# Kernel tuning notes

Hardware: AMD Instinct MI355X
Metric: run time of the kernel (lower is better)

## Reference

```python
import jax, jax.numpy as jnp
import numpy as np

N, D, E = 50000, 128, 800000


def setup_inputs() -> dict:
    key = jax.random.key(0)
    ks = jax.random.split(key, 12)
    x0 = jax.random.normal(ks[0], (N, D), dtype=jnp.float32)
    x1 = jax.random.normal(ks[1], (N, D), dtype=jnp.float32)
    edge_index = jax.random.randint(ks[2], (2, E), 0, N, dtype=jnp.int64)
    s = 0.05
    W1 = jax.random.normal(ks[3], (D, D), dtype=jnp.float32) * s
    b1 = jax.random.normal(ks[4], (D,), dtype=jnp.float32) * s
    W2 = jax.random.normal(ks[5], (D, D), dtype=jnp.float32) * s
    b2 = jax.random.normal(ks[6], (D,), dtype=jnp.float32) * s
    a1_w = jax.random.normal(ks[7], (D,), dtype=jnp.float32) * s
    a1_b = jax.random.normal(ks[8], (), dtype=jnp.float32) * s
    a2_w = jax.random.normal(ks[9], (D,), dtype=jnp.float32) * s
    a2_b = jax.random.normal(ks[10], (), dtype=jnp.float32) * s
    return {"x0": x0, "x1": x1, "edge_index": edge_index,
            "W1": W1, "b1": b1, "W2": W2, "b2": b2,
            "a1_w": a1_w, "a1_b": a1_b, "a2_w": a2_w, "a2_b": a2_b}


def reference(x0, x1, edge_index, W1, b1, W2, b2, a1_w, a1_b, a2_w, a2_b):
    # LeakyReLU(0.2) applied to both projections
    lrelu = lambda v: jnp.where(v >= 0, v, 0.2 * v)
    x0_i = lrelu(x0 @ W1.T + b1)          # [N, D]
    x0_j = lrelu(x0 @ W2.T + b2)          # [N, D]
    a1 = x0_i @ a1_w + a1_b               # [N]
    a2 = x0_j @ a2_w + a2_b               # [N]
    src, dst = edge_index[0], edge_index[1]
    # sigmoid(a_1 + a_2.T) evaluated only at the sparse edge indices
    att = jax.nn.sigmoid(a1[src] + a2[dst])            # [E]
    msg = att[:, None] * x0_j[dst]                     # [E, D]
    out = jax.ops.segment_sum(msg, src, num_segments=x0.shape[0])  # sparse.mm
    return out + x0
```

## Files before the change

### kernel.cpp

```cpp
#include <hip/hip_runtime.h>
#include <hip/hip_bf16.h>

typedef unsigned int u32;
typedef unsigned short u16;

#define DIM 128
#define LWS 136
#define CHUNK 2048

typedef __bf16 bfrag __attribute__((ext_vector_type(8)));
typedef float  facc  __attribute__((ext_vector_type(4)));

__device__ __forceinline__ float2 bfpair(u32 u) {
    union { u32 i; float f; } lo, hi;
    lo.i = (u & 0xFFFFu) << 16;
    hi.i = u & 0xFFFF0000u;
    return make_float2(lo.f, hi.f);
}
__device__ __forceinline__ float bf1(u16 h) {
    union { u32 i; float f; } a; a.i = ((u32)h) << 16; return a.f;
}
__device__ __forceinline__ u16 f2bf(float f) {
    __hip_bfloat16 h = __float2bfloat16(f);
    return *reinterpret_cast<u16*>(&h);
}
__device__ __forceinline__ u32 packbf(float x, float y) {
    return (u32)f2bf(x) | ((u32)f2bf(y) << 16);
}
__device__ __forceinline__ float ldfr(const void* p, int i, bool isbf) {
    return isbf ? bf1(((const u16*)p)[i]) : ((const float*)p)[i];
}

__global__ __launch_bounds__(64) void sniff_kernel(const u32* __restrict__ x0w,
                                                   const int* __restrict__ eiw,
                                                   int* __restrict__ flags) {
    int l = threadIdx.x;
    u32 w = x0w[l];
    u32 ef = (w >> 7) & 0xFF;
    bool inr = (ef >= 99 && ef <= 141);
    unsigned long long m1 = __ballot(inr);
    bool zodd = (eiw[2 * l + 1] == 0);
    unsigned long long m2 = __ballot(zodd);
    if (l == 0) {
        flags[0] = (__popcll(m1) >= 48) ? 1 : 0;
        flags[1] = (__popcll(m2) >= 32) ? 1 : 0;
    }
}

__global__ __launch_bounds__(256) void cvt_kernel(
    const float* __restrict__ x0, const float* __restrict__ W1,
    const float* __restrict__ W2, u16* __restrict__ x0c, u16* __restrict__ Wc,
    const int* __restrict__ flags, int nx)
{
    if (flags[0] != 0) return;
    int i = blockIdx.x * 256 + threadIdx.x;
    if (i >= nx + 4096) return;
    const float* src; u16* dst; int c;
    if (i < nx) { src = x0; dst = x0c; c = i; }
    else {
        int j = i - nx;
        src = (j < 2048) ? W1 : W2;
        dst = Wc + ((j < 2048) ? 0 : 16384);
        c = j & 2047;
    }
    float4 f0 = ((const float4*)src)[c * 2];
    float4 f1 = ((const float4*)src)[c * 2 + 1];
    uint4 u = make_uint4(packbf(f0.x, f0.y), packbf(f0.z, f0.w),
                         packbf(f1.x, f1.y), packbf(f1.z, f1.w));
    ((uint4*)dst)[c] = u;
}

__global__ __launch_bounds__(256) void proj_kernel(
    const void* __restrict__ x0v, const u16* __restrict__ x0c,
    const void* __restrict__ W1v, const void* __restrict__ b1v,
    const void* __restrict__ W2v, const void* __restrict__ b2v,
    const void* __restrict__ a1wv, const void* __restrict__ a1bv,
    const void* __restrict__ a2wv, const void* __restrict__ a2bv,
    const u16* __restrict__ Wc,
    u16* __restrict__ xj, float* __restrict__ a1, float* __restrict__ a2,
    const int* __restrict__ flags, int n, int nchunk, int bpg)
{
    __shared__ u16 lw[128 * LWS];

    const bool isbf = flags[0] != 0;
    const int t   = threadIdx.x;
    const int grp = blockIdx.x / bpg;
    const int cb  = blockIdx.x % bpg;

    const u16* x0s  = isbf ? (const u16*)x0v : x0c;
    const u16* Ws   = isbf ? (const u16*)(grp ? W2v : W1v) : (Wc + grp * 16384);
    const void* bv  = grp ? b2v  : b1v;
    const void* awv = grp ? a2wv : a1wv;
    const void* abv = grp ? a2bv : a1bv;
    float* aout     = grp ? a2   : a1;

    for (int j = t; j < 2048; j += 256) {
        int r = j >> 4, c = j & 15;
        *(uint4*)(lw + (size_t)r * LWS + c * 8) =
            *(const uint4*)(Ws + (size_t)r * DIM + c * 8);
    }
    __syncthreads();

    const int wid = t >> 6, l = t & 63;
    const int chunk = cb * 4 + wid;
    if (chunk >= nchunk) return;
    const int r0 = chunk * 32;
    const int lr = l & 15;
    const int q  = l >> 4;

    bfrag a[2][4];
    #pragma unroll
    for (int rt = 0; rt < 2; ++rt) {
        int row = min(r0 + rt * 16 + lr, n - 1);
        #pragma unroll
        for (int k = 0; k < 4; ++k) {
            const uint4* p = (const uint4*)(x0s + (size_t)row * DIM + k * 32 + q * 8);
            a[rt][k] = __builtin_bit_cast(bfrag, *p);
        }
    }

    facc acc[2][8];
    #pragma unroll
    for (int rt = 0; rt < 2; ++rt)
        #pragma unroll
        for (int ct = 0; ct < 8; ++ct)
            acc[rt][ct] = (facc){0.f, 0.f, 0.f, 0.f};

    #pragma unroll
    for (int ct = 0; ct < 8; ++ct) {
        bfrag bb[4];
        const u16* lrow = lw + (size_t)(ct * 16 + lr) * LWS;
        #pragma unroll
        for (int k = 0; k < 4; ++k)
            bb[k] = *(const bfrag*)(lrow + k * 32 + q * 8);
        #pragma unroll
        for (int rt = 0; rt < 2; ++rt)
            #pragma unroll
            for (int k = 0; k < 4; ++k)
                acc[rt][ct] = __builtin_amdgcn_mfma_f32_16x16x32_bf16(
                    a[rt][k], bb[k], acc[rt][ct], 0, 0, 0);
    }

    float s[2][4] = {{0.f,0.f,0.f,0.f},{0.f,0.f,0.f,0.f}};
    #pragma unroll
    for (int ct = 0; ct < 8; ++ct) {
        float bc  = ldfr(bv,  ct * 16 + lr, isbf);
        float awc = ldfr(awv, ct * 16 + lr, isbf);
        #pragma unroll
        for (int rt = 0; rt < 2; ++rt)
            #pragma unroll
            for (int reg = 0; reg < 4; ++reg) {
                float v = acc[rt][ct][reg] + bc;
                v = v >= 0.f ? v : 0.2f * v;
                int row = r0 + rt * 16 + q * 4 + reg;
                if (grp && row < n)
                    xj[(size_t)row * DIM + ct * 16 + lr] = f2bf(v);
                s[rt][reg] = fmaf(v, awc, s[rt][reg]);
            }
    }
    #pragma unroll
    for (int off = 1; off < 16; off <<= 1)
        #pragma unroll
        for (int rt = 0; rt < 2; ++rt)
            #pragma unroll
            for (int reg = 0; reg < 4; ++reg)
                s[rt][reg] += __shfl_xor(s[rt][reg], off);
    if (lr == 0) {
        float ab = ldfr(abv, 0, isbf);
        #pragma unroll
        for (int rt = 0; rt < 2; ++rt)
            #pragma unroll
            for (int reg = 0; reg < 4; ++reg) {
                int row = r0 + rt * 16 + q * 4 + reg;
                if (row < n) aout[row] = s[rt][reg] + ab;
            }
    }
}

__global__ __launch_bounds__(256) void countH_kernel(
    const int* __restrict__ ei, u32* __restrict__ keys0,
    int* __restrict__ cnt, const int* __restrict__ flags, int ne, int nblk)
{
    __shared__ int h[256];
    const int b = blockIdx.x, t = threadIdx.x;
    h[t] = 0;
    __syncthreads();
    const bool i64 = flags[1] != 0;
    const int base = b * CHUNK;
    #pragma unroll
    for (int r = 0; r < CHUNK / 256; ++r) {
        int i = base + r * 256 + t;
        if (i < ne) {
            int src = i64 ? ei[2 * i] : ei[i];
            int dst = i64 ? ei[2 * (ne + i)] : ei[ne + i];
            u32 key = ((u32)src << 16) | (u32)dst;
            keys0[i] = key;
            atomicAdd(&h[key >> 24], 1);
        }
    }
    __syncthreads();
    cnt[t * nblk + b] = h[t];
}

__global__ __launch_bounds__(256) void scan1_kernel(
    const int* __restrict__ cnt, int* __restrict__ off,
    int* __restrict__ tot, int nblk)
{
    __shared__ int v[512];
    const int d = blockIdx.x, t = threadIdx.x;
    int c0 = (t < nblk) ? cnt[d * nblk + t] : 0;
    int c1 = (t + 256 < nblk) ? cnt[d * nblk + t + 256] : 0;
    v[t] = c0; v[t + 256] = c1;
    __syncthreads();
    for (int s = 1; s < 512; s <<= 1) {
        int a0 = v[t],      b0 = (t >= s) ? v[t - s] : 0;
        int a1 = v[t + 256], b1 = (t + 256 >= s) ? v[t + 256 - s] : 0;
        __syncthreads();
        v[t] = a0 + b0; v[t + 256] = a1 + b1;
        __syncthreads();
    }
    if (t < nblk)       off[d * nblk + t]       = v[t] - c0;
    if (t + 256 < nblk) off[d * nblk + t + 256] = v[t + 256] - c1;
    if (t == 0) tot[d] = v[511];
}

__global__ __launch_bounds__(256) void scan2_kernel(
    const int* __restrict__ tot, int* __restrict__ basev)
{
    __shared__ int v[256];
    const int t = threadIdx.x;
    int c = tot[t];
    v[t] = c;
    __syncthreads();
    for (int s = 1; s < 256; s <<= 1) {
        int a = v[t], b = (t >= s) ? v[t - s] : 0;
        __syncthreads();
        v[t] = a + b;
        __syncthreads();
    }
    basev[t] = v[t] - c;
}

__global__ __launch_bounds__(256) void reorderH_kernel(
    const u32* __restrict__ kin, u32* __restrict__ kout,
    const int* __restrict__ off, const int* __restrict__ basev,
    int ne, int nblk)
{
    __shared__ int boff[256];
    __shared__ int bcnt[256];
    const int b = blockIdx.x, t = threadIdx.x;
    const int base = b * CHUNK;
    boff[t] = basev[t] + off[t * nblk + b];
    bcnt[t] = 0;
    __syncthreads();
    #pragma unroll
    for (int r = 0; r < CHUNK / 256; ++r) {
        int i = base + r * 256 + t;
        if (i < ne) {
            u32 key = kin[i];
            int d = key >> 24;
            int rk = atomicAdd(&bcnt[d], 1);
            kout[boff[d] + rk] = key;
        }
    }
}

__global__ __launch_bounds__(256) void bucket_kernel(
    const u32* __restrict__ keys1, const int* __restrict__ basev,
    const int* __restrict__ tot, const float* __restrict__ a1,
    const float* __restrict__ a2, int* __restrict__ ptr,
    u32* __restrict__ sorted, int n)
{
    __shared__ int cnt[256];
    __shared__ int sc[256];
    __shared__ int cur[256];
    const int b = blockIdx.x, t = threadIdx.x;
    const int base = basev[b];
    const int size = tot[b];
    cnt[t] = 0;
    __syncthreads();
    for (int i = t; i < size; i += 256)
        atomicAdd(&cnt[(keys1[base + i] >> 16) & 0xFF], 1);
    __syncthreads();
    int c = cnt[t];
    sc[t] = c;
    __syncthreads();
    for (int s = 1; s < 256; s <<= 1) {
        int a = sc[t], add = (t >= s) ? sc[t - s] : 0;
        __syncthreads();
        sc[t] = a + add;
        __syncthreads();
    }
    int ex = sc[t] - c;
    cur[t] = ex;
    int sg = (b << 8) + t;
    if (sg <= n) ptr[sg] = base + ex;
    __syncthreads();
    for (int i = t; i < size; i += 256) {
        u32 key = keys1[base + i];
        int j   = (key >> 16) & 0xFF;
        int rk  = atomicAdd(&cur[j], 1);
        int src = (int)(key >> 16);
        int dst = (int)(key & 0xFFFFu);
        float av  = a1[src] + a2[dst];
        float att = 1.0f / (1.0f + __expf(-av));
        u32 a16 = (u32)lrintf(att * 65535.0f);
        sorted[base + rk] = (a16 << 16) | (u32)dst;
    }
}

#define ATTDEC(r) ((float)((r) >> 16) * (1.0f / 65535.0f))

__global__ __launch_bounds__(256) void gather_kernel(
    const int* __restrict__ ptr, const u32* __restrict__ sorted,
    const u32* __restrict__ xjw, const void* __restrict__ x0v,
    void* __restrict__ outv, const int* __restrict__ flags, int n)
{
    const bool bf16 = flags[0] != 0;
    int s = blockIdx.x * 4 + (threadIdx.x >> 6);
    int l = threadIdx.x & 63;
    if (s >= n) return;

    float2 acc0, acc1;
    if (bf16) acc0 = bfpair(((const u32*)x0v)[(size_t)s * 64 + l]);
    else      acc0 = ((const float2*)x0v)[(size_t)s * 64 + l];
    acc1 = make_float2(0.f, 0.f);

    int k = ptr[s], end = ptr[s + 1];

    while (k + 16 <= end) {
        u32 r[16];
        #pragma unroll
        for (int j = 0; j < 16; ++j) r[j] = sorted[k + j];
        u32 w[16];
        #pragma unroll
        for (int j = 0; j < 16; ++j) w[j] = xjw[(size_t)(r[j] & 0xFFFFu) * 64 + l];
        #pragma unroll
        for (int j = 0; j < 16; ++j) {
            float att = ATTDEC(r[j]);
            float2 xv = bfpair(w[j]);
            if (j & 1) { acc1.x = fmaf(att, xv.x, acc1.x);
                         acc1.y = fmaf(att, xv.y, acc1.y); }
            else       { acc0.x = fmaf(att, xv.x, acc0.x);
                         acc0.y = fmaf(att, xv.y, acc0.y); }
        }
        k += 16;
    }
    if (k + 8 <= end) {
        u32 r[8];
        #pragma unroll
        for (int j = 0; j < 8; ++j) r[j] = sorted[k + j];
        u32 w[8];
        #pragma unroll
        for (int j = 0; j < 8; ++j) w[j] = xjw[(size_t)(r[j] & 0xFFFFu) * 64 + l];
        #pragma unroll
        for (int j = 0; j < 8; ++j) {
            float att = ATTDEC(r[j]);
            float2 xv = bfpair(w[j]);
            if (j & 1) { acc1.x = fmaf(att, xv.x, acc1.x);
                         acc1.y = fmaf(att, xv.y, acc1.y); }
            else       { acc0.x = fmaf(att, xv.x, acc0.x);
                         acc0.y = fmaf(att, xv.y, acc0.y); }
        }
        k += 8;
    }
    if (k + 4 <= end) {
        u32 r[4];
        #pragma unroll
        for (int j = 0; j < 4; ++j) r[j] = sorted[k + j];
        u32 w[4];
        #pragma unroll
        for (int j = 0; j < 4; ++j) w[j] = xjw[(size_t)(r[j] & 0xFFFFu) * 64 + l];
        #pragma unroll
        for (int j = 0; j < 4; ++j) {
            float att = ATTDEC(r[j]);
            float2 xv = bfpair(w[j]);
            if (j & 1) { acc1.x = fmaf(att, xv.x, acc1.x);
                         acc1.y = fmaf(att, xv.y, acc1.y); }
            else       { acc0.x = fmaf(att, xv.x, acc0.x);
                         acc0.y = fmaf(att, xv.y, acc0.y); }
        }
        k += 4;
    }
    for (; k < end; ++k) {
        u32 cur = sorted[k];
        float att = ATTDEC(cur);
        float2 xv = bfpair(xjw[(size_t)(cur & 0xFFFFu) * 64 + l]);
        acc0.x = fmaf(att, xv.x, acc0.x);
        acc0.y = fmaf(att, xv.y, acc0.y);
    }
    acc0.x += acc1.x;
    acc0.y += acc1.y;

    if (bf16) ((u32*)outv)[(size_t)s * 64 + l] = packbf(acc0.x, acc0.y);
    else      ((float2*)outv)[(size_t)s * 64 + l] = acc0;
}

extern "C" void kernel_launch(void* const* d_in, const int* in_sizes, int n_in,
                              void* d_out, int out_size, void* d_ws, size_t ws_size,
                              hipStream_t stream)
{
    const void* x0  = d_in[0];
    const int*  ei  = (const int*)d_in[2];
    const void* W1  = d_in[3];
    const void* b1  = d_in[4];
    const void* W2  = d_in[5];
    const void* b2  = d_in[6];
    const void* a1w = d_in[7];
    const void* a1b = d_in[8];
    const void* a2w = d_in[9];
    const void* a2b = d_in[10];

    const int n = in_sizes[0] / DIM;
    const int e = in_sizes[2] / 2;
    const int nblk = (e + CHUNK - 1) / CHUNK;

    char* ws = (char*)d_ws;
    int* flags = (int*)ws;
    size_t off = 1024;
    u16* xj = (u16*)(ws + off);
    off += (size_t)n * DIM * sizeof(u16);   off = (off + 255) & ~(size_t)255;
    u16* x0c = (u16*)(ws + off);
    off += (size_t)n * DIM * sizeof(u16);   off = (off + 255) & ~(size_t)255;
    u16* Wc = (u16*)(ws + off);
    off += (size_t)2 * 16384 * sizeof(u16); off = (off + 255) & ~(size_t)255;
    float* a1 = (float*)(ws + off);
    off += (size_t)n * sizeof(float);       off = (off + 255) & ~(size_t)255;
    float* a2 = (float*)(ws + off);
    off += (size_t)n * sizeof(float);       off = (off + 255) & ~(size_t)255;
    u32* keys0 = (u32*)(ws + off);
    off += (size_t)e * sizeof(u32);         off = (off + 255) & ~(size_t)255;
    u32* keys1 = (u32*)(ws + off);
    off += (size_t)e * sizeof(u32);         off = (off + 255) & ~(size_t)255;
    int* cntH = (int*)(ws + off);
    off += (size_t)256 * nblk * sizeof(int); off = (off + 255) & ~(size_t)255;
    int* offH = (int*)(ws + off);
    off += (size_t)256 * nblk * sizeof(int); off = (off + 255) & ~(size_t)255;
    int* totH = (int*)(ws + off);  off += 1024;
    int* baseH = (int*)(ws + off); off += 1024;
    int* ptr = (int*)(ws + off);
    off += (size_t)(n + 1) * sizeof(int);   off = (off + 255) & ~(size_t)255;
    u32* sorted = (u32*)(ws + off);

    sniff_kernel<<<1, 64, 0, stream>>>((const u32*)x0, ei, flags);

    const int nx = n * DIM / 8;
    const int cblocks = (nx + 4096 + 255) / 256;
    cvt_kernel<<<cblocks, 256, 0, stream>>>((const float*)x0, (const float*)W1,
        (const float*)W2, x0c, Wc, flags, nx);

    const int nchunk = (n + 31) / 32;
    const int bpg = (nchunk + 3) / 4;
    proj_kernel<<<2 * bpg, 256, 0, stream>>>(x0, x0c, W1, b1, W2, b2, a1w, a1b,
        a2w, a2b, Wc, xj, a1, a2, flags, n, nchunk, bpg);

    countH_kernel<<<nblk, 256, 0, stream>>>(ei, keys0, cntH, flags, e, nblk);
    scan1_kernel<<<256, 256, 0, stream>>>(cntH, offH, totH, nblk);
    scan2_kernel<<<1, 256, 0, stream>>>(totH, baseH);
    reorderH_kernel<<<nblk, 256, 0, stream>>>(keys0, keys1, offH, baseH, e, nblk);
    const int nbucket = (n >> 8) + 1;
    bucket_kernel<<<nbucket, 256, 0, stream>>>(keys1, baseH, totH, a1, a2,
                                               ptr, sorted, n);

    int gblocks = (n + 3) / 4;
    gather_kernel<<<gblocks, 256, 0, stream>>>(ptr, sorted, (const u32*)xj,
                                               x0, d_out, flags, n);
}
```

Measured before the change: 197.6 us.

## Merge independent pipeline stages into shared launches to cut kernel count

Fuses the bf16 conversion with the edge histogram count into one grid, fuses the per-digit scan with the projection GEMM into one grid, and drops the single-block second scan by recomputing the 256-entry prefix sum redundantly inside reorder and bucket blocks. This removes three launches and the serialization between independent stages, so they can occupy the GPU concurrently. In exchange every reorder and bucket block repeats a small 256-element scan, and the fused kernels carry the larger shared-memory footprint of the projection path, which may lower occupancy for the histogram and scan blocks.

```diff
diff --git a/kernel.cpp b/kernel.cpp
--- a/kernel.cpp
+++ b/kernel.cpp
@@ -47,146 +47,41 @@
     }
 }
 
-__global__ __launch_bounds__(256) void cvt_kernel(
+__global__ __launch_bounds__(256) void cvt_count_kernel(
     const float* __restrict__ x0, const float* __restrict__ W1,
     const float* __restrict__ W2, u16* __restrict__ x0c, u16* __restrict__ Wc,
-    const int* __restrict__ flags, int nx)
-{
-    if (flags[0] != 0) return;
-    int i = blockIdx.x * 256 + threadIdx.x;
-    if (i >= nx + 4096) return;
-    const float* src; u16* dst; int c;
-    if (i < nx) { src = x0; dst = x0c; c = i; }
-    else {
-        int j = i - nx;
-        src = (j < 2048) ? W1 : W2;
-        dst = Wc + ((j < 2048) ? 0 : 16384);
-        c = j & 2047;
-    }
-    float4 f0 = ((const float4*)src)[c * 2];
-    float4 f1 = ((const float4*)src)[c * 2 + 1];
-    uint4 u = make_uint4(packbf(f0.x, f0.y), packbf(f0.z, f0.w),
-                         packbf(f1.x, f1.y), packbf(f1.z, f1.w));
-    ((uint4*)dst)[c] = u;
-}
-
-__global__ __launch_bounds__(256) void proj_kernel(
-    const void* __restrict__ x0v, const u16* __restrict__ x0c,
-    const void* __restrict__ W1v, const void* __restrict__ b1v,
-    const void* __restrict__ W2v, const void* __restrict__ b2v,
-    const void* __restrict__ a1wv, const void* __restrict__ a1bv,
-    const void* __restrict__ a2wv, const void* __restrict__ a2bv,
-    const u16* __restrict__ Wc,
-    u16* __restrict__ xj, float* __restrict__ a1, float* __restrict__ a2,
-    const int* __restrict__ flags, int n, int nchunk, int bpg)
-{
-    __shared__ u16 lw[128 * LWS];
-
-    const bool isbf = flags[0] != 0;
-    const int t   = threadIdx.x;
-    const int grp = blockIdx.x / bpg;
-    const int cb  = blockIdx.x % bpg;
-
-    const u16* x0s  = isbf ? (const u16*)x0v : x0c;
-    const u16* Ws   = isbf ? (const u16*)(grp ? W2v : W1v) : (Wc + grp * 16384);
-    const void* bv  = grp ? b2v  : b1v;
-    const void* awv = grp ? a2wv : a1wv;
-    const void* abv = grp ? a2bv : a1bv;
-    float* aout     = grp ? a2   : a1;
-
-    for (int j = t; j < 2048; j += 256) {
-        int r = j >> 4, c = j & 15;
-        *(uint4*)(lw + (size_t)r * LWS + c * 8) =
-            *(const uint4*)(Ws + (size_t)r * DIM + c * 8);
-    }
-    __syncthreads();
-
-    const int wid = t >> 6, l = t & 63;
-    const int chunk = cb * 4 + wid;
-    if (chunk >= nchunk) return;
-    const int r0 = chunk * 32;
-    const int lr = l & 15;
-    const int q  = l >> 4;
-
-    bfrag a[2][4];
-    #pragma unroll
-    for (int rt = 0; rt < 2; ++rt) {
-        int row = min(r0 + rt * 16 + lr, n - 1);
-        #pragma unroll
-        for (int k = 0; k < 4; ++k) {
-            const uint4* p = (const uint4*)(x0s + (size_t)row * DIM + k * 32 + q * 8);
-            a[rt][k] = __builtin_bit_cast(bfrag, *p);
-        }
-    }
-
-    facc acc[2][8];
-    #pragma unroll
-    for (int rt = 0; rt < 2; ++rt)
-        #pragma unroll
-        for (int ct = 0; ct < 8; ++ct)
-            acc[rt][ct] = (facc){0.f, 0.f, 0.f, 0.f};
-
-    #pragma unroll
-    for (int ct = 0; ct < 8; ++ct) {
-        bfrag bb[4];
-        const u16* lrow = lw + (size_t)(ct * 16 + lr) * LWS;
-        #pragma unroll
-        for (int k = 0; k < 4; ++k)
-            bb[k] = *(const bfrag*)(lrow + k * 32 + q * 8);
-        #pragma unroll
-        for (int rt = 0; rt < 2; ++rt)
-            #pragma unroll
-            for (int k = 0; k < 4; ++k)
-                acc[rt][ct] = __builtin_amdgcn_mfma_f32_16x16x32_bf16(
-                    a[rt][k], bb[k], acc[rt][ct], 0, 0, 0);
-    }
-
-    float s[2][4] = {{0.f,0.f,0.f,0.f},{0.f,0.f,0.f,0.f}};
-    #pragma unroll
-    for (int ct = 0; ct < 8; ++ct) {
-        float bc  = ldfr(bv,  ct * 16 + lr, isbf);
-        float awc = ldfr(awv, ct * 16 + lr, isbf);
-        #pragma unroll
-        for (int rt = 0; rt < 2; ++rt)
-            #pragma unroll
-            for (int reg = 0; reg < 4; ++reg) {
-                float v = acc[rt][ct][reg] + bc;
-                v = v >= 0.f ? v : 0.2f * v;
-                int row = r0 + rt * 16 + q * 4 + reg;
-                if (grp && row < n)
-                    xj[(size_t)row * DIM + ct * 16 + lr] = f2bf(v);
-                s[rt][reg] = fmaf(v, awc, s[rt][reg]);
-            }
-    }
-    #pragma unroll
-    for (int off = 1; off < 16; off <<= 1)
-        #pragma unroll
-        for (int rt = 0; rt < 2; ++rt)
-            #pragma unroll
-            for (int reg = 0; reg < 4; ++reg)
-                s[rt][reg] += __shfl_xor(s[rt][reg], off);
-    if (lr == 0) {
-        float ab = ldfr(abv, 0, isbf);
-        #pragma unroll
-        for (int rt = 0; rt < 2; ++rt)
-            #pragma unroll
-            for (int reg = 0; reg < 4; ++reg) {
-                int row = r0 + rt * 16 + q * 4 + reg;
-                if (row < n) aout[row] = s[rt][reg] + ab;
-            }
-    }
-}
-
-__global__ __launch_bounds__(256) void countH_kernel(
-    const int* __restrict__ ei, u32* __restrict__ keys0,
-    int* __restrict__ cnt, const int* __restrict__ flags, int ne, int nblk)
+    const int* __restrict__ ei, u32* __restrict__ keys0, int* __restrict__ cnt,
+    const int* __restrict__ flags, int nx, int ne, int nblk, int ncvt)
 {
     __shared__ int h[256];
     const int b = blockIdx.x, t = threadIdx.x;
+
+    if (b < ncvt) {
+        if (flags[0] != 0) return;
+        int i = b * 256 + t;
+        if (i >= nx + 4096) return;
+        const float* src; u16* dst; int c;
+        if (i < nx) { src = x0; dst = x0c; c = i; }
+        else {
+            int j = i - nx;
+            src = (j < 2048) ? W1 : W2;
+            dst = Wc + ((j < 2048) ? 0 : 16384);
+            c = j & 2047;
+        }
+        float4 f0 = ((const float4*)src)[c * 2];
+        float4 f1 = ((const float4*)src)[c * 2 + 1];
+        uint4 u = make_uint4(packbf(f0.x, f0.y), packbf(f0.z, f0.w),
+                             packbf(f1.x, f1.y), packbf(f1.z, f1.w));
+        ((uint4*)dst)[c] = u;
+        return;
+    }
+
+    const int hb = b - ncvt;
+    if (hb >= nblk) return;
     h[t] = 0;
     __syncthreads();
     const bool i64 = flags[1] != 0;
-    const int base = b * CHUNK;
+    const int base = hb * CHUNK;
     #pragma unroll
     for (int r = 0; r < CHUNK / 256; ++r) {
         int i = base + r * 256 + t;
@@ -199,86 +94,197 @@
         }
     }
     __syncthreads();
-    cnt[t * nblk + b] = h[t];
-}
-
-__global__ __launch_bounds__(256) void scan1_kernel(
-    const int* __restrict__ cnt, int* __restrict__ off,
-    int* __restrict__ tot, int nblk)
-{
+    cnt[t * nblk + hb] = h[t];
+}
+
+__global__ __launch_bounds__(256) void proj_scan_kernel(
+    const void* __restrict__ x0v, const u16* __restrict__ x0c,
+    const void* __restrict__ W1v, const void* __restrict__ b1v,
+    const void* __restrict__ W2v, const void* __restrict__ b2v,
+    const void* __restrict__ a1wv, const void* __restrict__ a1bv,
+    const void* __restrict__ a2wv, const void* __restrict__ a2bv,
+    const u16* __restrict__ Wc,
+    u16* __restrict__ xj, float* __restrict__ a1, float* __restrict__ a2,
+    const int* __restrict__ cnt, int* __restrict__ off, int* __restrict__ tot,
+    const int* __restrict__ flags, int n, int nchunk, int bpg, int nblk)
+{
+    __shared__ u16 lw[128 * LWS];
     __shared__ int v[512];
-    const int d = blockIdx.x, t = threadIdx.x;
-    int c0 = (t < nblk) ? cnt[d * nblk + t] : 0;
-    int c1 = (t + 256 < nblk) ? cnt[d * nblk + t + 256] : 0;
-    v[t] = c0; v[t + 256] = c1;
-    __syncthreads();
-    for (int s = 1; s < 512; s <<= 1) {
-        int a0 = v[t],      b0 = (t >= s) ? v[t - s] : 0;
-        int a1 = v[t + 256], b1 = (t + 256 >= s) ? v[t + 256 - s] : 0;
-        __syncthreads();
-        v[t] = a0 + b0; v[t + 256] = a1 + b1;
-        __syncthreads();
-    }
-    if (t < nblk)       off[d * nblk + t]       = v[t] - c0;
-    if (t + 256 < nblk) off[d * nblk + t + 256] = v[t + 256] - c1;
-    if (t == 0) tot[d] = v[511];
-}
-
-__global__ __launch_bounds__(256) void scan2_kernel(
-    const int* __restrict__ tot, int* __restrict__ basev)
-{
-    __shared__ int v[256];
-    const int t = threadIdx.x;
-    int c = tot[t];
-    v[t] = c;
-    __syncthreads();
-    for (int s = 1; s < 256; s <<= 1) {
-        int a = v[t], b = (t >= s) ? v[t - s] : 0;
-        __syncthreads();
-        v[t] = a + b;
-        __syncthreads();
-    }
-    basev[t] = v[t] - c;
+    const int b = blockIdx.x, t = threadIdx.x;
+
+    if (b < 256) {
+        const int d = b;
+        int c0 = (t < nblk) ? cnt[d * nblk + t] : 0;
+        int c1 = (t + 256 < nblk) ? cnt[d * nblk + t + 256] : 0;
+        v[t] = c0; v[t + 256] = c1;
+        __syncthreads();
+        for (int s = 1; s < 512; s <<= 1) {
+            int a0 = v[t],       b0 = (t >= s) ? v[t - s] : 0;
+            int a1v = v[t + 256], b1v = (t + 256 >= s) ? v[t + 256 - s] : 0;
+            __syncthreads();
+            v[t] = a0 + b0; v[t + 256] = a1v + b1v;
+            __syncthreads();
+        }
+        if (t < nblk)       off[d * nblk + t]       = v[t] - c0;
+        if (t + 256 < nblk) off[d * nblk + t + 256] = v[t + 256] - c1;
+        if (t == 0) tot[d] = v[511];
+        return;
+    }
+
+    const bool isbf = flags[0] != 0;
+    const int pid = b - 256;
+    const int grp = pid / bpg;
+    const int cb  = pid % bpg;
+
+    const u16* x0s  = isbf ? (const u16*)x0v : x0c;
+    const u16* Ws   = isbf ? (const u16*)(grp ? W2v : W1v) : (Wc + grp * 16384);
+    const void* bv  = grp ? b2v  : b1v;
+    const void* awv = grp ? a2wv : a1wv;
+    const void* abv = grp ? a2bv : a1bv;
+    float* aout     = grp ? a2   : a1;
+
+    for (int j = t; j < 2048; j += 256) {
+        int r = j >> 4, c = j & 15;
+        *(uint4*)(lw + (size_t)r * LWS + c * 8) =
+            *(const uint4*)(Ws + (size_t)r * DIM + c * 8);
+    }
+    __syncthreads();
+
+    const int wid = t >> 6, l = t & 63;
+    const int chunk = cb * 4 + wid;
+    if (chunk >= nchunk) return;
+    const int r0 = chunk * 32;
+    const int lr = l & 15;
+    const int q  = l >> 4;
+
+    bfrag a[2][4];
+    #pragma unroll
+    for (int rt = 0; rt < 2; ++rt) {
+        int row = min(r0 + rt * 16 + lr, n - 1);
+        #pragma unroll
+        for (int k = 0; k < 4; ++k) {
+            const uint4* p = (const uint4*)(x0s + (size_t)row * DIM + k * 32 + q * 8);
+            a[rt][k] = __builtin_bit_cast(bfrag, *p);
+        }
+    }
+
+    facc acc[2][8];
+    #pragma unroll
+    for (int rt = 0; rt < 2; ++rt)
+        #pragma unroll
+        for (int ct = 0; ct < 8; ++ct)
+            acc[rt][ct] = (facc){0.f, 0.f, 0.f, 0.f};
+
+    #pragma unroll
+    for (int ct = 0; ct < 8; ++ct) {
+        bfrag bb[4];
+        const u16* lrow = lw + (size_t)(ct * 16 + lr) * LWS;
+        #pragma unroll
+        for (int k = 0; k < 4; ++k)
+            bb[k] = *(const bfrag*)(lrow + k * 32 + q * 8);
+        #pragma unroll
+        for (int rt = 0; rt < 2; ++rt)
+            #pragma unroll
+            for (int k = 0; k < 4; ++k)
+                acc[rt][ct] = __builtin_amdgcn_mfma_f32_16x16x32_bf16(
+                    a[rt][k], bb[k], acc[rt][ct], 0, 0, 0);
+    }
+
+    float s[2][4] = {{0.f,0.f,0.f,0.f},{0.f,0.f,0.f,0.f}};
+    #pragma unroll
+    for (int ct = 0; ct < 8; ++ct) {
+        float bc  = ldfr(bv,  ct * 16 + lr, isbf);
+        float awc = ldfr(awv, ct * 16 + lr, isbf);
+        #pragma unroll
+        for (int rt = 0; rt < 2; ++rt)
+            #pragma unroll
+            for (int reg = 0; reg < 4; ++reg) {
+                float vv = acc[rt][ct][reg] + bc;
+                vv = vv >= 0.f ? vv : 0.2f * vv;
+                int row = r0 + rt * 16 + q * 4 + reg;
+                if (grp && row < n)
+                    xj[(size_t)row * DIM + ct * 16 + lr] = f2bf(vv);
+                s[rt][reg] = fmaf(vv, awc, s[rt][reg]);
+            }
+    }
+    #pragma unroll
+    for (int o = 1; o < 16; o <<= 1)
+        #pragma unroll
+        for (int rt = 0; rt < 2; ++rt)
+            #pragma unroll
+            for (int reg = 0; reg < 4; ++reg)
+                s[rt][reg] += __shfl_xor(s[rt][reg], o);
+    if (lr == 0) {
+        float ab = ldfr(abv, 0, isbf);
+        #pragma unroll
+        for (int rt = 0; rt < 2; ++rt)
+            #pragma unroll
+            for (int reg = 0; reg < 4; ++reg) {
+                int row = r0 + rt * 16 + q * 4 + reg;
+                if (row < n) aout[row] = s[rt][reg] + ab;
+            }
+    }
 }
 
 __global__ __launch_bounds__(256) void reorderH_kernel(
     const u32* __restrict__ kin, u32* __restrict__ kout,
-    const int* __restrict__ off, const int* __restrict__ basev,
+    const int* __restrict__ off, const int* __restrict__ tot,
     int ne, int nblk)
 {
     __shared__ int boff[256];
-    __shared__ int bcnt[256];
+    __shared__ int sv[256];
     const int b = blockIdx.x, t = threadIdx.x;
+    int c = tot[t];
+    sv[t] = c;
+    __syncthreads();
+    for (int s = 1; s < 256; s <<= 1) {
+        int a = sv[t], add = (t >= s) ? sv[t - s] : 0;
+        __syncthreads();
+        sv[t] = a + add;
+        __syncthreads();
+    }
+    boff[t] = (sv[t] - c) + off[t * nblk + b];
+    sv[t] = 0;
+    __syncthreads();
     const int base = b * CHUNK;
-    boff[t] = basev[t] + off[t * nblk + b];
-    bcnt[t] = 0;
-    __syncthreads();
     #pragma unroll
     for (int r = 0; r < CHUNK / 256; ++r) {
         int i = base + r * 256 + t;
         if (i < ne) {
             u32 key = kin[i];
             int d = key >> 24;
-            int rk = atomicAdd(&bcnt[d], 1);
+            int rk = atomicAdd(&sv[d], 1);
             kout[boff[d] + rk] = key;
         }
     }
 }
 
 __global__ __launch_bounds__(256) void bucket_kernel(
-    const u32* __restrict__ keys1, const int* __restrict__ basev,
-    const int* __restrict__ tot, const float* __restrict__ a1,
-    const float* __restrict__ a2, int* __restrict__ ptr,
-    u32* __restrict__ sorted, int n)
+    const u32* __restrict__ keys1, const int* __restrict__ tot,
+    const float* __restrict__ a1, const float* __restrict__ a2,
+    int* __restrict__ ptr, u32* __restrict__ sorted, int n)
 {
     __shared__ int cnt[256];
     __shared__ int sc[256];
     __shared__ int cur[256];
+    __shared__ int bas[256];
     const int b = blockIdx.x, t = threadIdx.x;
-    const int base = basev[b];
+
+    int c0 = tot[t];
+    sc[t] = c0;
+    __syncthreads();
+    for (int s = 1; s < 256; s <<= 1) {
+        int a = sc[t], add = (t >= s) ? sc[t - s] : 0;
+        __syncthreads();
+        sc[t] = a + add;
+        __syncthreads();
+    }
+    bas[t] = sc[t] - c0;
+    cnt[t] = 0;
+    __syncthreads();
+    const int base = bas[b];
     const int size = tot[b];
-    cnt[t] = 0;
-    __syncthreads();
+
     for (int i = t; i < size; i += 256)
         atomicAdd(&cnt[(keys1[base + i] >> 16) & 0xFF], 1);
     __syncthreads();
@@ -437,7 +443,6 @@
     int* offH = (int*)(ws + off);
     off += (size_t)256 * nblk * sizeof(int); off = (off + 255) & ~(size_t)255;
     int* totH = (int*)(ws + off);  off += 1024;
-    int* baseH = (int*)(ws + off); off += 1024;
     int* ptr = (int*)(ws + off);
     off += (size_t)(n + 1) * sizeof(int);   off = (off + 255) & ~(size_t)255;
     u32* sorted = (u32*)(ws + off);
@@ -445,21 +450,21 @@
     sniff_kernel<<<1, 64, 0, stream>>>((const u32*)x0, ei, flags);
 
     const int nx = n * DIM / 8;
-    const int cblocks = (nx + 4096 + 255) / 256;
-    cvt_kernel<<<cblocks, 256, 0, stream>>>((const float*)x0, (const float*)W1,
-        (const float*)W2, x0c, Wc, flags, nx);
+    const int ncvt = (nx + 4096 + 255) / 256;
+    cvt_count_kernel<<<ncvt + nblk, 256, 0, stream>>>((const float*)x0,
+        (const float*)W1, (const float*)W2, x0c, Wc, ei, keys0, cntH,
+        flags, nx, e, nblk, ncvt);
 
     const int nchunk = (n + 31) / 32;
     const int bpg = (nchunk + 3) / 4;
-    proj_kernel<<<2 * bpg, 256, 0, stream>>>(x0, x0c, W1, b1, W2, b2, a1w, a1b,
-        a2w, a2b, Wc, xj, a1, a2, flags, n, nchunk, bpg);
-
-    countH_kernel<<<nblk, 256, 0, stream>>>(ei, keys0, cntH, flags, e, nblk);
-    scan1_kernel<<<256, 256, 0, stream>>>(cntH, offH, totH, nblk);
-    scan2_kernel<<<1, 256, 0, stream>>>(totH, baseH);
-    reorderH_kernel<<<nblk, 256, 0, stream>>>(keys0, keys1, offH, baseH, e, nblk);
+    proj_scan_kernel<<<256 + 2 * bpg, 256, 0, stream>>>(x0, x0c, W1, b1, W2, b2,
+        a1w, a1b, a2w, a2b, Wc, xj, a1, a2, cntH, offH, totH, flags,
+        n, nchunk, bpg, nblk);
+
+    reorderH_kernel<<<nblk, 256, 0, stream>>>(keys0, keys1, offH, totH, e, nblk);
+
     const int nbucket = (n >> 8) + 1;
-    bucket_kernel<<<nbucket, 256, 0, stream>>>(keys1, baseH, totH, a1, a2,
+    bucket_kernel<<<nbucket, 256, 0, stream>>>(keys1, totH, a1, a2,
                                                ptr, sorted, n);
 
     int gblocks = (n + 3) / 4;
```

Measured after the change: 191.8 us. -2.9%, faster.
